# Optimization experiments

Measured on AMD Instinct MI355X. Metric: run time of the kernel, lower is better.

Reference implementation:

```python
import jax, jax.numpy as jnp
import numpy as np

B, N, WIDTH, HEADS = 4, 2048, 1024, 16
HEAD_DIM = WIDTH // HEADS  # 64


def setup_inputs() -> dict:
    key = jax.random.key(0)
    k1, k2, k3 = jax.random.split(key, 3)
    x = jax.random.normal(k1, (B, N, WIDTH), dtype=jnp.float32)
    # Linear weights stored as [in, out] (torch stores [out, in]; math y = x @ W_in_out + b)
    w_qkv = jax.random.normal(k2, (WIDTH, 3 * WIDTH), dtype=jnp.float32) * (1.0 / np.sqrt(WIDTH))
    b_qkv = jnp.zeros((3 * WIDTH,), dtype=jnp.float32)
    w_proj = jax.random.normal(k3, (WIDTH, WIDTH), dtype=jnp.float32) * (1.0 / np.sqrt(WIDTH))
    b_proj = jnp.zeros((WIDTH,), dtype=jnp.float32)
    return {"x": x, "w_qkv": w_qkv, "b_qkv": b_qkv, "w_proj": w_proj, "b_proj": b_proj}


def reference(x, w_qkv, b_qkv, w_proj, b_proj):
    bs, n_ctx, width = x.shape
    qkv = x @ w_qkv + b_qkv                      # [b, n, 3*width]
    attn_ch = HEAD_DIM                            # width // heads
    scale = 1.0 / np.sqrt(np.sqrt(attn_ch))       # 1/sqrt(sqrt(d)) applied to q and k
    qkv = qkv.reshape(bs, n_ctx, HEADS, 3 * attn_ch)
    q, k, v = jnp.split(qkv, 3, axis=-1)          # each [b, n, h, d]
    weight = jnp.einsum('bthc,bshc->bhts', q * scale, k * scale)
    weight = jax.nn.softmax(weight, axis=-1)
    out = jnp.einsum('bhts,bshc->bthc', weight, v).reshape(bs, n_ctx, -1)
    return out @ w_proj + b_proj
```

## Files before the change

kernel.cpp:

```cpp
#include <hip/hip_runtime.h>

typedef __attribute__((ext_vector_type(8))) short bf16x8;
typedef __attribute__((ext_vector_type(4))) float f32x4;
typedef __attribute__((ext_vector_type(8))) unsigned short u16x8;
typedef __attribute__((ext_vector_type(4))) unsigned short u16x4;
typedef __attribute__((ext_vector_type(2))) unsigned u32x2;

__device__ __forceinline__ unsigned short f2bf(float f) {
  unsigned u = __builtin_bit_cast(unsigned, f);
  return (unsigned short)((u + 0x7fffu + ((u >> 16) & 1u)) >> 16);
}

__device__ __forceinline__ unsigned cvt_pk_bf16(float lo, float hi) {
  unsigned r;
  asm("v_cvt_pk_bf16_f32 %0, %1, %2" : "=v"(r) : "v"(lo), "v"(hi));
  return r;
}

__device__ __forceinline__ void gl_lds16(const void* g, void* l) {
  __builtin_amdgcn_global_load_lds((const __attribute__((address_space(1))) unsigned*)g,
                                   (__attribute__((address_space(3))) unsigned*)l, 16, 0, 0);
}

__global__ __launch_bounds__(256) void k_cvt(const float* __restrict__ x,
                                             unsigned short* __restrict__ xb) {
  int i = blockIdx.x * 256 + threadIdx.x;
  const float4* s = (const float4*)x;
  float4 a = s[2 * i], b = s[2 * i + 1];
  u16x8 o;
  o[0] = f2bf(a.x); o[1] = f2bf(a.y); o[2] = f2bf(a.z); o[3] = f2bf(a.w);
  o[4] = f2bf(b.x); o[5] = f2bf(b.y); o[6] = f2bf(b.z); o[7] = f2bf(b.w);
  *(u16x8*)(xb + 8 * (size_t)i) = o;
}

__global__ __launch_bounds__(256) void k_wT(const float* __restrict__ w,
                                            unsigned short* __restrict__ wT,
                                            int Nn, int Kk) {
  __shared__ float tile[32][33];
  const int k0 = blockIdx.x * 32, n0 = blockIdx.y * 32;
  const int t = threadIdx.x;
  const int i = t >> 3, j = (t & 7) * 4;
  float4 v = *(const float4*)(w + (size_t)(k0 + i) * Nn + n0 + j);
  tile[i][j] = v.x; tile[i][j + 1] = v.y; tile[i][j + 2] = v.z; tile[i][j + 3] = v.w;
  __syncthreads();
  const int n = i, k4 = j;
  u16x4 o;
  o[0] = f2bf(tile[k4 + 0][n]); o[1] = f2bf(tile[k4 + 1][n]);
  o[2] = f2bf(tile[k4 + 2][n]); o[3] = f2bf(tile[k4 + 3][n]);
  *(u16x4*)(wT + (size_t)(n0 + n) * Kk + k0 + k4) = o;
}

template <int EPI>
__global__ __launch_bounds__(256) void k_gemm(const unsigned short* __restrict__ A,
                                              const unsigned short* __restrict__ Bt,
                                              const float* __restrict__ bias, int Nx,
                                              float* __restrict__ outF,
                                              unsigned short* __restrict__ Qb,
                                              unsigned short* __restrict__ Kb,
                                              unsigned short* __restrict__ Vb) {
  __shared__ unsigned short As[128 * 32];
  __shared__ unsigned short Bs[128 * 32];
  const int t = threadIdx.x;
  const int brow = blockIdx.x * 128, bcol = blockIdx.y * 128;
  const int lane = t & 63, wid = t >> 6;
  const int wr = (wid >> 1) * 64, wc = (wid & 1) * 64;
  const int g = lane >> 4, qr = lane & 15;
  const f32x4 fzero = {0.f, 0.f, 0.f, 0.f};
  f32x4 acc[4][4];
#pragma unroll
  for (int i = 0; i < 4; ++i)
#pragma unroll
    for (int n = 0; n < 4; ++n) acc[i][n] = fzero;
  const unsigned short* Ag = A + (size_t)(brow + (t >> 2)) * 1024 + (t & 3) * 8;
  const unsigned short* Bg = Bt + (size_t)(bcol + (t >> 2)) * 1024 + (t & 3) * 8;
  unsigned short* Asl = As + t * 8;
  unsigned short* Bsl = Bs + t * 8;
  for (int kt = 0; kt < 32; ++kt) {
    const int k0 = kt * 32;
    gl_lds16(Ag + k0, Asl);
    gl_lds16(Ag + 64 * 1024 + k0, Asl + 2048);
    gl_lds16(Bg + k0, Bsl);
    gl_lds16(Bg + 64 * 1024 + k0, Bsl + 2048);
    __syncthreads();
    bf16x8 a[4], b[4];
#pragma unroll
    for (int i = 0; i < 4; ++i) a[i] = *(const bf16x8*)&As[(wr + i * 16 + qr) * 32 + g * 8];
#pragma unroll
    for (int n = 0; n < 4; ++n) b[n] = *(const bf16x8*)&Bs[(wc + n * 16 + qr) * 32 + g * 8];
#pragma unroll
    for (int i = 0; i < 4; ++i)
#pragma unroll
      for (int n = 0; n < 4; ++n)
        acc[i][n] = __builtin_amdgcn_mfma_f32_16x16x32_bf16(a[i], b[n], acc[i][n], 0, 0, 0);
    __syncthreads();
  }
#pragma unroll
  for (int i = 0; i < 4; ++i) {
#pragma unroll
    for (int n = 0; n < 4; ++n) {
      const int col = bcol + wc + n * 16 + qr;
      const float bv = bias[col];
      float v4[4];
#pragma unroll
      for (int r = 0; r < 4; ++r) v4[r] = acc[i][n][r] + bv;
      const int row0 = brow + wr + i * 16 + g * 4;
      if constexpr (EPI == 0) {
#pragma unroll
        for (int r = 0; r < 4; ++r) outF[(size_t)(row0 + r) * Nx + col] = v4[r];
      } else {
        const int bb = row0 >> 11, tkn0 = row0 & 2047;
        const unsigned c = (unsigned)col;
        const unsigned h = c / 192u;
        const unsigned rem = c - h * 192u;
        const unsigned which = rem >> 6, d = rem & 63u;
        if (which == 2u) {
          u16x4 pk;
#pragma unroll
          for (int r = 0; r < 4; ++r) pk[r] = f2bf(v4[r]);
          *(u16x4*)&Vb[(size_t)(((unsigned)bb * 16u + h) * 64u + d) * 2048u + (unsigned)tkn0] = pk;
        } else {
          const float sc = (which == 0u) ? (0.35355339059327373f * 1.4426950408889634f)
                                         : 0.35355339059327373f;
          unsigned short* dst = (which == 0u) ? Qb : Kb;
#pragma unroll
          for (int r = 0; r < 4; ++r)
            dst[(size_t)(((unsigned)bb * 16u + h) * 2048u + (unsigned)(tkn0 + r)) * 64u + d] =
                f2bf(v4[r] * sc);
        }
      }
    }
  }
}

__global__ __launch_bounds__(512, 6) void k_attn(const unsigned short* __restrict__ Qb,
                                                 const unsigned short* __restrict__ Kb,
                                                 const unsigned short* __restrict__ Vt,
                                                 unsigned short* __restrict__ Ao) {
  __shared__ unsigned short Kl[2][64][64];
  __shared__ unsigned short Vl[2][64][64];
  __shared__ unsigned short Pl[8][16][72];
  const int bid = blockIdx.x;
  const int bh = (bid & 7) * 8 + ((bid >> 3) >> 4);
  const int qt = (bid >> 3) & 15;
  const int t = threadIdx.x, lane = t & 63, w = t >> 6;
  const int g = lane >> 4, q = lane & 15;
  const int q0 = qt * 128 + w * 16;
  const unsigned short* Qbase = Qb + ((size_t)bh * 2048 + q0) * 64;
  const char* Kg = (const char*)(Kb + (size_t)bh * 2048 * 64);
  const char* Vg = (const char*)(Vt + (size_t)bh * 64 * 2048);
  const int lr = lane >> 3, lc = lane & 7;
  const int swz = (lc ^ lr) << 4;
  const char* Ksrc = Kg + (size_t)(8 * w + lr) * 128 + swz;
  const char* Vsrc = Vg + (size_t)(8 * w + lr) * 4096 + swz;
  unsigned short* Kd0 = &Kl[0][8 * w][0] + lane * 8;
  unsigned short* Kd1 = &Kl[1][8 * w][0] + lane * 8;
  unsigned short* Vd0 = &Vl[0][8 * w][0] + lane * 8;
  unsigned short* Vd1 = &Vl[1][8 * w][0] + lane * 8;

  bf16x8 qf0 = *(const bf16x8*)(Qbase + (size_t)q * 64 + g * 8);
  bf16x8 qf1 = *(const bf16x8*)(Qbase + (size_t)q * 64 + 32 + g * 8);
  const f32x4 fzero = {0.f, 0.f, 0.f, 0.f};
  f32x4 o[4];
#pragma unroll
  for (int i = 0; i < 4; ++i) o[i] = fzero;
  float m = -1e30f, l = 0.f;

  gl_lds16(Ksrc, Kd0);
  gl_lds16(Vsrc, Vd0);
  __syncthreads();

  for (int it = 0; it < 32; ++it) {
    const int cur = it & 1;
    if (it < 31) {
      const size_t nx = (size_t)(it + 1);
      gl_lds16(Ksrc + nx * 8192, cur ? Kd0 : Kd1);
      gl_lds16(Vsrc + nx * 128, cur ? Vd0 : Vd1);
    }
    f32x4 s[4];
    __builtin_amdgcn_s_setprio(1);
#pragma unroll
    for (int kf = 0; kf < 4; ++kf) {
      const int row = kf * 16 + q;
      const char* kp = (const char*)&Kl[cur][row][0];
      const int sw = (row & 7) << 4;
      bf16x8 kaL = *(const bf16x8*)(kp + ((g * 16) ^ sw));
      bf16x8 kaH = *(const bf16x8*)(kp + ((64 + g * 16) ^ sw));
      s[kf] = __builtin_amdgcn_mfma_f32_16x16x32_bf16(kaL, qf0, fzero, 0, 0, 0);
      s[kf] = __builtin_amdgcn_mfma_f32_16x16x32_bf16(kaH, qf1, s[kf], 0, 0, 0);
    }
    __builtin_amdgcn_s_setprio(0);
    float mt = fmaxf(fmaxf(fmaxf(s[0][0], s[0][1]), fmaxf(s[0][2], s[0][3])),
                     fmaxf(fmaxf(s[1][0], s[1][1]), fmaxf(s[1][2], s[1][3])));
    mt = fmaxf(mt, fmaxf(fmaxf(fmaxf(s[2][0], s[2][1]), fmaxf(s[2][2], s[2][3])),
                         fmaxf(fmaxf(s[3][0], s[3][1]), fmaxf(s[3][2], s[3][3]))));
    mt = fmaxf(mt, __shfl_xor(mt, 16));
    mt = fmaxf(mt, __shfl_xor(mt, 32));
    if (!__all(mt - m <= 11.5f)) {
      const float mnew = fmaxf(m, mt);
      const float al = __builtin_amdgcn_exp2f(m - mnew);
      const float a0 = __shfl(al, 4 * g + 0), a1 = __shfl(al, 4 * g + 1);
      const float a2 = __shfl(al, 4 * g + 2), a3 = __shfl(al, 4 * g + 3);
#pragma unroll
      for (int i = 0; i < 4; ++i) { o[i][0] *= a0; o[i][1] *= a1; o[i][2] *= a2; o[i][3] *= a3; }
      l *= al;
      m = mnew;
    }
    unsigned short* Pw = &Pl[w][q][0];
    float ts = 0.f;
#pragma unroll
    for (int kf = 0; kf < 4; ++kf) {
      const float e0 = __builtin_amdgcn_exp2f(s[kf][0] - m);
      const float e1 = __builtin_amdgcn_exp2f(s[kf][1] - m);
      const float e2 = __builtin_amdgcn_exp2f(s[kf][2] - m);
      const float e3 = __builtin_amdgcn_exp2f(s[kf][3] - m);
      ts += (e0 + e1) + (e2 + e3);
      u32x2 pk;
      pk[0] = cvt_pk_bf16(e0, e1);
      pk[1] = cvt_pk_bf16(e2, e3);
      *(u32x2*)(Pw + (8 * kf + 2 * g) * 2) = pk;
    }
    ts += __shfl_xor(ts, 16);
    ts += __shfl_xor(ts, 32);
    l += ts;
    asm volatile("" ::: "memory");
    const bf16x8 pa0 = *(const bf16x8*)&Pl[w][q][g * 8];
    const bf16x8 pa1 = *(const bf16x8*)&Pl[w][q][32 + g * 8];
    __builtin_amdgcn_s_setprio(1);
#pragma unroll
    for (int dblk = 0; dblk < 4; ++dblk) {
      const int row = dblk * 16 + q;
      const char* vp = (const char*)&Vl[cur][row][0];
      const int sw = (row & 7) << 4;
      bf16x8 vL = *(const bf16x8*)(vp + ((g * 16) ^ sw));
      bf16x8 vH = *(const bf16x8*)(vp + ((64 + g * 16) ^ sw));
      o[dblk] = __builtin_amdgcn_mfma_f32_16x16x32_bf16(pa0, vL, o[dblk], 0, 0, 0);
      o[dblk] = __builtin_amdgcn_mfma_f32_16x16x32_bf16(pa1, vH, o[dblk], 0, 0, 0);
    }
    __builtin_amdgcn_s_setprio(0);
    __syncthreads();
  }
  const float linv = 1.0f / l;
  float rr[4];
  rr[0] = __shfl(linv, 4 * g + 0); rr[1] = __shfl(linv, 4 * g + 1);
  rr[2] = __shfl(linv, 4 * g + 2); rr[3] = __shfl(linv, 4 * g + 3);
  const int bb = bh >> 4, hh = bh & 15;
  unsigned short* ob = Ao + ((size_t)bb * 2048 + q0 + 4 * g) * 1024 + hh * 64 + q;
#pragma unroll
  for (int dblk = 0; dblk < 4; ++dblk)
#pragma unroll
    for (int r = 0; r < 4; ++r)
      ob[(size_t)r * 1024 + dblk * 16] = f2bf(o[dblk][r] * rr[r]);
}

extern "C" void kernel_launch(void* const* d_in, const int* in_sizes, int n_in,
                              void* d_out, int out_size, void* d_ws, size_t ws_size,
                              hipStream_t stream) {
  const float* x = (const float*)d_in[0];
  const float* w_qkv = (const float*)d_in[1];
  const float* b_qkv = (const float*)d_in[2];
  const float* w_proj = (const float*)d_in[3];
  const float* b_proj = (const float*)d_in[4];
  float* out = (float*)d_out;
  char* ws = (char*)d_ws;
  unsigned short* xb = (unsigned short*)(ws);
  unsigned short* wqkvT = (unsigned short*)(ws + 16777216);
  unsigned short* wprojT = (unsigned short*)(ws + 23068672);
  unsigned short* Qb = (unsigned short*)(ws + 25165824);
  unsigned short* Kb = (unsigned short*)(ws + 41943040);
  unsigned short* Vt = (unsigned short*)(ws + 58720256);
  unsigned short* Ao = xb;

  hipLaunchKernelGGL(k_cvt, dim3(4096), dim3(256), 0, stream, x, xb);
  hipLaunchKernelGGL(k_wT, dim3(32, 96), dim3(256), 0, stream, w_qkv, wqkvT, 3072, 1024);
  hipLaunchKernelGGL(k_wT, dim3(32, 32), dim3(256), 0, stream, w_proj, wprojT, 1024, 1024);
  hipLaunchKernelGGL((k_gemm<1>), dim3(64, 24), dim3(256), 0, stream,
                     xb, wqkvT, b_qkv, 3072, (float*)nullptr, Qb, Kb, Vt);
  hipLaunchKernelGGL(k_attn, dim3(1024), dim3(512), 0, stream, Qb, Kb, Vt, Ao);
  hipLaunchKernelGGL((k_gemm<0>), dim3(64, 8), dim3(256), 0, stream,
                     Ao, wprojT, b_proj, 1024, out,
                     (unsigned short*)nullptr, (unsigned short*)nullptr, (unsigned short*)nullptr);
}
```

Measured before the change: 209.6 us.

## Process two query groups per attention wave and remap GEMM blocks across XCDs

The attention kernel now runs 4 waves of 256 threads, each handling 32 query rows as two 16-row groups. Each K/V fragment read from LDS is then reused for twice as many MFMAs, and each wave stages twice the K/V rows. The GEMM grid becomes 1D, with block IDs remapped so consecutive tiles land on the same XCD for better L2 locality. The cost is higher register pressure in attention and fewer waves per block to hide latency.

```diff
diff --git a/kernel.cpp b/kernel.cpp
--- a/kernel.cpp
+++ b/kernel.cpp
@@ -54,6 +54,7 @@
 __global__ __launch_bounds__(256) void k_gemm(const unsigned short* __restrict__ A,
                                               const unsigned short* __restrict__ Bt,
                                               const float* __restrict__ bias, int Nx,
+                                              int MT,
                                               float* __restrict__ outF,
                                               unsigned short* __restrict__ Qb,
                                               unsigned short* __restrict__ Kb,
@@ -61,7 +62,9 @@
   __shared__ unsigned short As[128 * 32];
   __shared__ unsigned short Bs[128 * 32];
   const int t = threadIdx.x;
-  const int brow = blockIdx.x * 128, bcol = blockIdx.y * 128;
+  const int nwg = gridDim.x;
+  const int wg = (blockIdx.x & 7) * (nwg >> 3) + (blockIdx.x >> 3);
+  const int brow = (wg % MT) * 128, bcol = (wg / MT) * 128;
   const int lane = t & 63, wid = t >> 6;
   const int wr = (wid >> 1) * 64, wc = (wid & 1) * 64;
   const int g = lane >> 4, qr = lane & 15;
@@ -132,51 +135,61 @@
   }
 }
 
-__global__ __launch_bounds__(512, 6) void k_attn(const unsigned short* __restrict__ Qb,
+__global__ __launch_bounds__(256, 3) void k_attn(const unsigned short* __restrict__ Qb,
                                                  const unsigned short* __restrict__ Kb,
                                                  const unsigned short* __restrict__ Vt,
                                                  unsigned short* __restrict__ Ao) {
   __shared__ unsigned short Kl[2][64][64];
   __shared__ unsigned short Vl[2][64][64];
-  __shared__ unsigned short Pl[8][16][72];
+  __shared__ unsigned short Pl[4][2][16][72];
   const int bid = blockIdx.x;
   const int bh = (bid & 7) * 8 + ((bid >> 3) >> 4);
   const int qt = (bid >> 3) & 15;
   const int t = threadIdx.x, lane = t & 63, w = t >> 6;
   const int g = lane >> 4, q = lane & 15;
-  const int q0 = qt * 128 + w * 16;
+  const int q0 = qt * 128 + w * 32;
   const unsigned short* Qbase = Qb + ((size_t)bh * 2048 + q0) * 64;
   const char* Kg = (const char*)(Kb + (size_t)bh * 2048 * 64);
   const char* Vg = (const char*)(Vt + (size_t)bh * 64 * 2048);
   const int lr = lane >> 3, lc = lane & 7;
   const int swz = (lc ^ lr) << 4;
-  const char* Ksrc = Kg + (size_t)(8 * w + lr) * 128 + swz;
-  const char* Vsrc = Vg + (size_t)(8 * w + lr) * 4096 + swz;
-  unsigned short* Kd0 = &Kl[0][8 * w][0] + lane * 8;
-  unsigned short* Kd1 = &Kl[1][8 * w][0] + lane * 8;
-  unsigned short* Vd0 = &Vl[0][8 * w][0] + lane * 8;
-  unsigned short* Vd1 = &Vl[1][8 * w][0] + lane * 8;
-
-  bf16x8 qf0 = *(const bf16x8*)(Qbase + (size_t)q * 64 + g * 8);
-  bf16x8 qf1 = *(const bf16x8*)(Qbase + (size_t)q * 64 + 32 + g * 8);
+  const char* Ks0 = Kg + (size_t)(16 * w + lr) * 128 + swz;
+  const char* Ks1 = Kg + (size_t)(16 * w + 8 + lr) * 128 + swz;
+  const char* Vs0 = Vg + (size_t)(16 * w + lr) * 4096 + swz;
+  const char* Vs1 = Vg + (size_t)(16 * w + 8 + lr) * 4096 + swz;
+  unsigned short* Kd[2], *Vd[2];
+  Kd[0] = &Kl[0][16 * w][0] + lane * 8;
+  Kd[1] = &Kl[1][16 * w][0] + lane * 8;
+  Vd[0] = &Vl[0][16 * w][0] + lane * 8;
+  Vd[1] = &Vl[1][16 * w][0] + lane * 8;
+
+#define STAGE(buf, it_)                                    \
+  do {                                                     \
+    gl_lds16(Ks0 + (size_t)(it_) * 8192, Kd[buf]);         \
+    gl_lds16(Ks1 + (size_t)(it_) * 8192, Kd[buf] + 512);   \
+    gl_lds16(Vs0 + (size_t)(it_) * 128, Vd[buf]);          \
+    gl_lds16(Vs1 + (size_t)(it_) * 128, Vd[buf] + 512);    \
+  } while (0)
+
+  bf16x8 qf[2][2];
+#pragma unroll
+  for (int G = 0; G < 2; ++G)
+#pragma unroll
+    for (int h = 0; h < 2; ++h)
+      qf[G][h] = *(const bf16x8*)(Qbase + (size_t)(G * 16 + q) * 64 + h * 32 + g * 8);
   const f32x4 fzero = {0.f, 0.f, 0.f, 0.f};
-  f32x4 o[4];
-#pragma unroll
-  for (int i = 0; i < 4; ++i) o[i] = fzero;
-  float m = -1e30f, l = 0.f;
-
-  gl_lds16(Ksrc, Kd0);
-  gl_lds16(Vsrc, Vd0);
+  f32x4 o0[4], o1[4];
+#pragma unroll
+  for (int i = 0; i < 4; ++i) { o0[i] = fzero; o1[i] = fzero; }
+  float m0 = -1e30f, l0 = 0.f, m1 = -1e30f, l1 = 0.f;
+
+  STAGE(0, 0);
   __syncthreads();
 
   for (int it = 0; it < 32; ++it) {
     const int cur = it & 1;
-    if (it < 31) {
-      const size_t nx = (size_t)(it + 1);
-      gl_lds16(Ksrc + nx * 8192, cur ? Kd0 : Kd1);
-      gl_lds16(Vsrc + nx * 128, cur ? Vd0 : Vd1);
-    }
-    f32x4 s[4];
+    if (it < 31) STAGE(cur ^ 1, it + 1);
+    f32x4 s0[4], s1[4];
     __builtin_amdgcn_s_setprio(1);
 #pragma unroll
     for (int kf = 0; kf < 4; ++kf) {
@@ -185,46 +198,87 @@
       const int sw = (row & 7) << 4;
       bf16x8 kaL = *(const bf16x8*)(kp + ((g * 16) ^ sw));
       bf16x8 kaH = *(const bf16x8*)(kp + ((64 + g * 16) ^ sw));
-      s[kf] = __builtin_amdgcn_mfma_f32_16x16x32_bf16(kaL, qf0, fzero, 0, 0, 0);
-      s[kf] = __builtin_amdgcn_mfma_f32_16x16x32_bf16(kaH, qf1, s[kf], 0, 0, 0);
+      s0[kf] = __builtin_amdgcn_mfma_f32_16x16x32_bf16(kaL, qf[0][0], fzero, 0, 0, 0);
+      s0[kf] = __builtin_amdgcn_mfma_f32_16x16x32_bf16(kaH, qf[0][1], s0[kf], 0, 0, 0);
+      s1[kf] = __builtin_amdgcn_mfma_f32_16x16x32_bf16(kaL, qf[1][0], fzero, 0, 0, 0);
+      s1[kf] = __builtin_amdgcn_mfma_f32_16x16x32_bf16(kaH, qf[1][1], s1[kf], 0, 0, 0);
     }
     __builtin_amdgcn_s_setprio(0);
-    float mt = fmaxf(fmaxf(fmaxf(s[0][0], s[0][1]), fmaxf(s[0][2], s[0][3])),
-                     fmaxf(fmaxf(s[1][0], s[1][1]), fmaxf(s[1][2], s[1][3])));
-    mt = fmaxf(mt, fmaxf(fmaxf(fmaxf(s[2][0], s[2][1]), fmaxf(s[2][2], s[2][3])),
-                         fmaxf(fmaxf(s[3][0], s[3][1]), fmaxf(s[3][2], s[3][3]))));
-    mt = fmaxf(mt, __shfl_xor(mt, 16));
-    mt = fmaxf(mt, __shfl_xor(mt, 32));
-    if (!__all(mt - m <= 11.5f)) {
-      const float mnew = fmaxf(m, mt);
-      const float al = __builtin_amdgcn_exp2f(m - mnew);
-      const float a0 = __shfl(al, 4 * g + 0), a1 = __shfl(al, 4 * g + 1);
-      const float a2 = __shfl(al, 4 * g + 2), a3 = __shfl(al, 4 * g + 3);
-#pragma unroll
-      for (int i = 0; i < 4; ++i) { o[i][0] *= a0; o[i][1] *= a1; o[i][2] *= a2; o[i][3] *= a3; }
-      l *= al;
-      m = mnew;
-    }
-    unsigned short* Pw = &Pl[w][q][0];
-    float ts = 0.f;
-#pragma unroll
-    for (int kf = 0; kf < 4; ++kf) {
-      const float e0 = __builtin_amdgcn_exp2f(s[kf][0] - m);
-      const float e1 = __builtin_amdgcn_exp2f(s[kf][1] - m);
-      const float e2 = __builtin_amdgcn_exp2f(s[kf][2] - m);
-      const float e3 = __builtin_amdgcn_exp2f(s[kf][3] - m);
-      ts += (e0 + e1) + (e2 + e3);
-      u32x2 pk;
-      pk[0] = cvt_pk_bf16(e0, e1);
-      pk[1] = cvt_pk_bf16(e2, e3);
-      *(u32x2*)(Pw + (8 * kf + 2 * g) * 2) = pk;
-    }
-    ts += __shfl_xor(ts, 16);
-    ts += __shfl_xor(ts, 32);
-    l += ts;
+    {
+      float mt = fmaxf(fmaxf(fmaxf(s0[0][0], s0[0][1]), fmaxf(s0[0][2], s0[0][3])),
+                       fmaxf(fmaxf(s0[1][0], s0[1][1]), fmaxf(s0[1][2], s0[1][3])));
+      mt = fmaxf(mt, fmaxf(fmaxf(fmaxf(s0[2][0], s0[2][1]), fmaxf(s0[2][2], s0[2][3])),
+                           fmaxf(fmaxf(s0[3][0], s0[3][1]), fmaxf(s0[3][2], s0[3][3]))));
+      mt = fmaxf(mt, __shfl_xor(mt, 16));
+      mt = fmaxf(mt, __shfl_xor(mt, 32));
+      if (!__all(mt - m0 <= 11.5f)) {
+        const float mnew = fmaxf(m0, mt);
+        const float al = __builtin_amdgcn_exp2f(m0 - mnew);
+        const float a0 = __shfl(al, 4 * g + 0), a1 = __shfl(al, 4 * g + 1);
+        const float a2 = __shfl(al, 4 * g + 2), a3 = __shfl(al, 4 * g + 3);
+#pragma unroll
+        for (int i = 0; i < 4; ++i) { o0[i][0] *= a0; o0[i][1] *= a1; o0[i][2] *= a2; o0[i][3] *= a3; }
+        l0 *= al;
+        m0 = mnew;
+      }
+      unsigned short* Pw = &Pl[w][0][q][0];
+      float ts = 0.f;
+#pragma unroll
+      for (int kf = 0; kf < 4; ++kf) {
+        const float e0 = __builtin_amdgcn_exp2f(s0[kf][0] - m0);
+        const float e1 = __builtin_amdgcn_exp2f(s0[kf][1] - m0);
+        const float e2 = __builtin_amdgcn_exp2f(s0[kf][2] - m0);
+        const float e3 = __builtin_amdgcn_exp2f(s0[kf][3] - m0);
+        ts += (e0 + e1) + (e2 + e3);
+        u32x2 pk;
+        pk[0] = cvt_pk_bf16(e0, e1);
+        pk[1] = cvt_pk_bf16(e2, e3);
+        *(u32x2*)(Pw + (8 * kf + 2 * g) * 2) = pk;
+      }
+      ts += __shfl_xor(ts, 16);
+      ts += __shfl_xor(ts, 32);
+      l0 += ts;
+    }
+    {
+      float mt = fmaxf(fmaxf(fmaxf(s1[0][0], s1[0][1]), fmaxf(s1[0][2], s1[0][3])),
+                       fmaxf(fmaxf(s1[1][0], s1[1][1]), fmaxf(s1[1][2], s1[1][3])));
+      mt = fmaxf(mt, fmaxf(fmaxf(fmaxf(s1[2][0], s1[2][1]), fmaxf(s1[2][2], s1[2][3])),
+                           fmaxf(fmaxf(s1[3][0], s1[3][1]), fmaxf(s1[3][2], s1[3][3]))));
+      mt = fmaxf(mt, __shfl_xor(mt, 16));
+      mt = fmaxf(mt, __shfl_xor(mt, 32));
+      if (!__all(mt - m1 <= 11.5f)) {
+        const float mnew = fmaxf(m1, mt);
+        const float al = __builtin_amdgcn_exp2f(m1 - mnew);
+        const float a0 = __shfl(al, 4 * g + 0), a1 = __shfl(al, 4 * g + 1);
+        const float a2 = __shfl(al, 4 * g + 2), a3 = __shfl(al, 4 * g + 3);
+#pragma unroll
+        for (int i = 0; i < 4; ++i) { o1[i][0] *= a0; o1[i][1] *= a1; o1[i][2] *= a2; o1[i][3] *= a3; }
+        l1 *= al;
+        m1 = mnew;
+      }
+      unsigned short* Pw = &Pl[w][1][q][0];
+      float ts = 0.f;
+#pragma unroll
+      for (int kf = 0; kf < 4; ++kf) {
+        const float e0 = __builtin_amdgcn_exp2f(s1[kf][0] - m1);
+        const float e1 = __builtin_amdgcn_exp2f(s1[kf][1] - m1);
+        const float e2 = __builtin_amdgcn_exp2f(s1[kf][2] - m1);
+        const float e3 = __builtin_amdgcn_exp2f(s1[kf][3] - m1);
+        ts += (e0 + e1) + (e2 + e3);
+        u32x2 pk;
+        pk[0] = cvt_pk_bf16(e0, e1);
+        pk[1] = cvt_pk_bf16(e2, e3);
+        *(u32x2*)(Pw + (8 * kf + 2 * g) * 2) = pk;
+      }
+      ts += __shfl_xor(ts, 16);
+      ts += __shfl_xor(ts, 32);
+      l1 += ts;
+    }
     asm volatile("" ::: "memory");
-    const bf16x8 pa0 = *(const bf16x8*)&Pl[w][q][g * 8];
-    const bf16x8 pa1 = *(const bf16x8*)&Pl[w][q][32 + g * 8];
+    const bf16x8 pa00 = *(const bf16x8*)&Pl[w][0][q][g * 8];
+    const bf16x8 pa01 = *(const bf16x8*)&Pl[w][0][q][32 + g * 8];
+    const bf16x8 pa10 = *(const bf16x8*)&Pl[w][1][q][g * 8];
+    const bf16x8 pa11 = *(const bf16x8*)&Pl[w][1][q][32 + g * 8];
     __builtin_amdgcn_s_setprio(1);
 #pragma unroll
     for (int dblk = 0; dblk < 4; ++dblk) {
@@ -233,23 +287,40 @@
       const int sw = (row & 7) << 4;
       bf16x8 vL = *(const bf16x8*)(vp + ((g * 16) ^ sw));
       bf16x8 vH = *(const bf16x8*)(vp + ((64 + g * 16) ^ sw));
-      o[dblk] = __builtin_amdgcn_mfma_f32_16x16x32_bf16(pa0, vL, o[dblk], 0, 0, 0);
-      o[dblk] = __builtin_amdgcn_mfma_f32_16x16x32_bf16(pa1, vH, o[dblk], 0, 0, 0);
+      o0[dblk] = __builtin_amdgcn_mfma_f32_16x16x32_bf16(pa00, vL, o0[dblk], 0, 0, 0);
+      o0[dblk] = __builtin_amdgcn_mfma_f32_16x16x32_bf16(pa01, vH, o0[dblk], 0, 0, 0);
+      o1[dblk] = __builtin_amdgcn_mfma_f32_16x16x32_bf16(pa10, vL, o1[dblk], 0, 0, 0);
+      o1[dblk] = __builtin_amdgcn_mfma_f32_16x16x32_bf16(pa11, vH, o1[dblk], 0, 0, 0);
     }
     __builtin_amdgcn_s_setprio(0);
     __syncthreads();
   }
-  const float linv = 1.0f / l;
-  float rr[4];
-  rr[0] = __shfl(linv, 4 * g + 0); rr[1] = __shfl(linv, 4 * g + 1);
-  rr[2] = __shfl(linv, 4 * g + 2); rr[3] = __shfl(linv, 4 * g + 3);
+#undef STAGE
   const int bb = bh >> 4, hh = bh & 15;
-  unsigned short* ob = Ao + ((size_t)bb * 2048 + q0 + 4 * g) * 1024 + hh * 64 + q;
-#pragma unroll
-  for (int dblk = 0; dblk < 4; ++dblk)
-#pragma unroll
-    for (int r = 0; r < 4; ++r)
-      ob[(size_t)r * 1024 + dblk * 16] = f2bf(o[dblk][r] * rr[r]);
+  {
+    const float linv = 1.0f / l0;
+    float rr[4];
+    rr[0] = __shfl(linv, 4 * g + 0); rr[1] = __shfl(linv, 4 * g + 1);
+    rr[2] = __shfl(linv, 4 * g + 2); rr[3] = __shfl(linv, 4 * g + 3);
+    unsigned short* ob = Ao + ((size_t)bb * 2048 + q0 + 4 * g) * 1024 + hh * 64 + q;
+#pragma unroll
+    for (int dblk = 0; dblk < 4; ++dblk)
+#pragma unroll
+      for (int r = 0; r < 4; ++r)
+        ob[(size_t)r * 1024 + dblk * 16] = f2bf(o0[dblk][r] * rr[r]);
+  }
+  {
+    const float linv = 1.0f / l1;
+    float rr[4];
+    rr[0] = __shfl(linv, 4 * g + 0); rr[1] = __shfl(linv, 4 * g + 1);
+    rr[2] = __shfl(linv, 4 * g + 2); rr[3] = __shfl(linv, 4 * g + 3);
+    unsigned short* ob = Ao + ((size_t)bb * 2048 + q0 + 16 + 4 * g) * 1024 + hh * 64 + q;
+#pragma unroll
+    for (int dblk = 0; dblk < 4; ++dblk)
+#pragma unroll
+      for (int r = 0; r < 4; ++r)
+        ob[(size_t)r * 1024 + dblk * 16] = f2bf(o1[dblk][r] * rr[r]);
+  }
 }
 
 extern "C" void kernel_launch(void* const* d_in, const int* in_sizes, int n_in,
@@ -273,10 +344,10 @@
   hipLaunchKernelGGL(k_cvt, dim3(4096), dim3(256), 0, stream, x, xb);
   hipLaunchKernelGGL(k_wT, dim3(32, 96), dim3(256), 0, stream, w_qkv, wqkvT, 3072, 1024);
   hipLaunchKernelGGL(k_wT, dim3(32, 32), dim3(256), 0, stream, w_proj, wprojT, 1024, 1024);
-  hipLaunchKernelGGL((k_gemm<1>), dim3(64, 24), dim3(256), 0, stream,
-                     xb, wqkvT, b_qkv, 3072, (float*)nullptr, Qb, Kb, Vt);
-  hipLaunchKernelGGL(k_attn, dim3(1024), dim3(512), 0, stream, Qb, Kb, Vt, Ao);
-  hipLaunchKernelGGL((k_gemm<0>), dim3(64, 8), dim3(256), 0, stream,
-                     Ao, wprojT, b_proj, 1024, out,
+  hipLaunchKernelGGL((k_gemm<1>), dim3(1536), dim3(256), 0, stream,
+                     xb, wqkvT, b_qkv, 3072, 64, (float*)nullptr, Qb, Kb, Vt);
+  hipLaunchKernelGGL(k_attn, dim3(1024), dim3(256), 0, stream, Qb, Kb, Vt, Ao);
+  hipLaunchKernelGGL((k_gemm<0>), dim3(512), dim3(256), 0, stream,
+                     Ao, wprojT, b_proj, 1024, 64, out,
                      (unsigned short*)nullptr, (unsigned short*)nullptr, (unsigned short*)nullptr);
 }
```

Result: slower. 224.5 us (+7.1%).
